# Optimization experiments

Hardware: AMD Instinct MI355X
Metric: run time of the kernel (lower is better)

Reference implementation:

```python
import jax, jax.numpy as jnp
import numpy as np

GN_EPS = 1e-5
GN_GROUPS = 8
KNN_EPS = 1e-8


def group_norm(x, w, b):
    # x: [B, C, N]
    B, C, N = x.shape
    xg = x.reshape(B, GN_GROUPS, C // GN_GROUPS, N)
    mu = jnp.mean(xg, axis=(2, 3), keepdims=True)
    var = jnp.var(xg, axis=(2, 3), keepdims=True)
    xg = (xg - mu) * jax.lax.rsqrt(var + GN_EPS)
    return xg.reshape(B, C, N) * w[None, :, None] + b[None, :, None]


def swish(x):
    return x * jax.nn.sigmoid(x)


def three_interpolate(points_coords, centers_coords, centers_features):
    # points_coords [B,3,N], centers_coords [B,3,M], centers_features [B,C,M]
    B, _, N = points_coords.shape
    C = centers_features.shape[1]
    p2 = jnp.sum(points_coords ** 2, axis=1)            # [B,N]
    c2 = jnp.sum(centers_coords ** 2, axis=1)           # [B,M]
    cross = jnp.einsum('bdn,bdm->bnm', points_coords, centers_coords)
    dist2 = p2[:, :, None] + c2[:, None, :] - 2.0 * cross  # [B,N,M] squared dists
    neg_d, idx = jax.lax.top_k(-dist2, 3)               # 3 smallest -> [B,N,3]
    d = -neg_d
    w = 1.0 / (d + KNN_EPS)
    w = w / jnp.sum(w, axis=-1, keepdims=True)          # [B,N,3]
    featsT = jnp.swapaxes(centers_features, 1, 2)       # [B,M,C]
    gathered = jnp.take_along_axis(featsT, idx.reshape(B, N * 3, 1), axis=1)
    gathered = gathered.reshape(B, N, 3, C)
    out = jnp.einsum('bnk,bnkc->bcn', w, gathered)      # [B,C,N]
    return out


def setup_inputs() -> dict:
    key = jax.random.key(0)
    ks = jax.random.split(key, 8)
    B, N, M = 8, 8192, 2048
    C_ctr, C_pts, D = 256, 128, 64
    Cin, C1, C2 = C_ctr + C_pts, 256, 256
    return {
        'points_coords': jax.random.normal(ks[0], (B, 3, N), jnp.float32),
        'centers_coords': jax.random.normal(ks[1], (B, 3, M), jnp.float32),
        'centers_features': jax.random.normal(ks[2], (B, C_ctr, M), jnp.float32),
        'points_features': jax.random.normal(ks[3], (B, C_pts, N), jnp.float32),
        'time_emb': jax.random.normal(ks[4], (B, D, 1), jnp.float32),
        'W1': jax.random.normal(ks[5], (C1, Cin), jnp.float32) * (1.0 / np.sqrt(Cin)),
        'b1': jnp.zeros((C1,), jnp.float32),
        'gn1_w': jnp.ones((C1,), jnp.float32),
        'gn1_b': jnp.zeros((C1,), jnp.float32),
        'W2': jax.random.normal(ks[6], (C2, C1), jnp.float32) * (1.0 / np.sqrt(C1)),
        'b2': jnp.zeros((C2,), jnp.float32),
        'gn2_w': jnp.ones((C2,), jnp.float32),
        'gn2_b': jnp.zeros((C2,), jnp.float32),
    }


def reference(points_coords, centers_coords, centers_features, points_features,
              time_emb, W1, b1, gn1_w, gn1_b, W2, b2, gn2_w, gn2_b):
    interp = three_interpolate(points_coords, centers_coords, centers_features)
    x = jnp.concatenate([interp, points_features], axis=1)  # [B, Cin, N]
    # SharedMLP layer 1: Conv1d(k=1) + GroupNorm(8) + Swish
    x = jnp.einsum('oc,bcn->bon', W1, x) + b1[None, :, None]
    x = swish(group_norm(x, gn1_w, gn1_b))
    # layer 2
    x = jnp.einsum('oc,bcn->bon', W2, x) + b2[None, :, None]
    x = swish(group_norm(x, gn2_w, gn2_b))
    N = points_coords.shape[-1]
    time_emb_exp = jnp.broadcast_to(time_emb[:, :, 0:1], time_emb.shape[:2] + (N,))
    return (x, points_coords, time_emb_exp)
```

## Files before the change

kernel.cpp:

```cpp
#include <hip/hip_runtime.h>
#include <hip/hip_bf16.h>
#include <float.h>

#define B_ 8
#define N_ 8192
#define M_ 2048
#define CC_ 256
#define CP_ 128
#define CIN_ 384
#define GRP_ 8

typedef __attribute__((ext_vector_type(8))) short short8;
typedef __attribute__((ext_vector_type(4))) short short4v;
typedef __attribute__((ext_vector_type(4))) float f32x4;

static __device__ __forceinline__ float bf2f(unsigned short u) {
  union { unsigned int i; float f; } v; v.i = ((unsigned int)u) << 16; return v.f;
}
static __device__ __forceinline__ unsigned short f2bf(float f) {
  union { float f; unsigned int i; } v; v.f = f;
  unsigned int u = v.i;
  unsigned int r = (u + 0x7FFFu + ((u >> 16) & 1u)) >> 16;
  return (unsigned short)r;
}
static __device__ __forceinline__ void gload16(const void* g, void* l) {
  __builtin_amdgcn_global_load_lds(
      (const __attribute__((address_space(1))) void*)g,
      (__attribute__((address_space(3))) void*)l, 16, 0, 0);
}

__global__ __launch_bounds__(256) void k_prep(
    const float* __restrict__ W1, const float* __restrict__ W2,
    short* __restrict__ W1b, short* __restrict__ W2b,
    const float* __restrict__ cf, short* __restrict__ FT,
    const float* __restrict__ pf, short* __restrict__ x0T) {
  __shared__ float tile[32][33];
  int bid = blockIdx.x;
  int t = threadIdx.x;
  if (bid < 384) {
    int i = bid * 256 + t;
    if (i < 256 * CIN_) W1b[i] = (short)f2bf(W1[i]);
    if (i < 256 * 256)  W2b[i] = (short)f2bf(W2[i]);
    return;
  }
  const float* in; short* out;
  int C, Nn, RS, coff, n0, c0, b;
  if (bid < 4480) {
    int q = bid - 384;
    in = cf; out = FT; C = CC_; Nn = M_; RS = CC_; coff = 0;
    n0 = (q & 63) * 32; c0 = ((q >> 6) & 7) * 32; b = q >> 9;
  } else {
    int q = bid - 4480;
    in = pf; out = x0T; C = CP_; Nn = N_; RS = CIN_; coff = 256;
    n0 = (q & 255) * 32; c0 = ((q >> 8) & 3) * 32; b = q >> 10;
  }
  const float* inb = in + (size_t)b * C * Nn;
  short* outb = out + (size_t)b * Nn * RS;
  int tx = t & 31, ty = t >> 5;
#pragma unroll
  for (int i = 0; i < 32; i += 8)
    tile[ty + i][tx] = inb[(size_t)(c0 + ty + i) * Nn + n0 + tx];
  __syncthreads();
#pragma unroll
  for (int i = 0; i < 32; i += 8)
    outb[(size_t)(n0 + ty + i) * RS + coff + c0 + tx] = (short)f2bf(tile[tx][ty + i]);
}

__global__ __launch_bounds__(256) void k_knn(
    const float* __restrict__ pc, const float* __restrict__ cc,
    int* __restrict__ idx, float* __restrict__ wts) {
  __shared__ __align__(16) float4 ctr[M_];
  __shared__ double mk[4][3][64];
  int b = blockIdx.y;
  int t = threadIdx.x;
  const float* ccb = cc + (size_t)b * 3 * M_;
  for (int i = t; i < M_; i += 256) {
    float x = ccb[i], y = ccb[M_ + i], z = ccb[2 * M_ + i];
    ctr[i] = make_float4(x, y, z, x * x + y * y + z * z);
  }
  __syncthreads();
  int wv = t >> 6, lane = t & 63;
  int n = blockIdx.x * 64 + lane;
  const float* pcb = pc + (size_t)b * 3 * N_;
  float px = pcb[n], py = pcb[N_ + n], pz = pcb[2 * N_ + n];
  float p2 = px * px + py * py + pz * pz;
  double k0 = __hiloint2double(0x7F7FFFFF, 0);
  double k1 = k0, k2 = k0;
  const float4* C = ctr + wv * 512;
  int mbase = wv * 512;
#pragma unroll 8
  for (int m = 0; m < 512; ++m) {
    float4 c = C[m];
    float dot = px * c.x;
    dot = __builtin_fmaf(py, c.y, dot);
    dot = __builtin_fmaf(pz, c.z, dot);
    float d = __builtin_fmaf(-2.f, dot, c.w) + p2;
    double key = __hiloint2double(__float_as_int(d), mbase + m);
    double n0 = fmin(key, k0);
    double n1 = fmin(fmax(key, k0), k1);
    double n2 = fmin(fmax(key, k1), k2);
    k0 = n0; k1 = n1; k2 = n2;
  }
  mk[wv][0][lane] = k0; mk[wv][1][lane] = k1; mk[wv][2][lane] = k2;
  __syncthreads();
  if (t < 64) {
#pragma unroll
    for (int w = 1; w < 4; ++w) {
#pragma unroll
      for (int j = 0; j < 3; ++j) {
        double key = mk[w][j][t];
        double n0 = fmin(key, k0);
        double n1 = fmin(fmax(key, k0), k1);
        double n2 = fmin(fmax(key, k1), k2);
        k0 = n0; k1 = n1; k2 = n2;
      }
    }
    float d0 = __int_as_float(__double2hiint(k0));
    float d1 = __int_as_float(__double2hiint(k1));
    float d2 = __int_as_float(__double2hiint(k2));
    float w0 = 1.f / (d0 + 1e-8f), w1 = 1.f / (d1 + 1e-8f), w2 = 1.f / (d2 + 1e-8f);
    float inv = 1.f / (w0 + w1 + w2);
    int bn = b * N_ + blockIdx.x * 64 + t;
    wts[bn] = w0 * inv; wts[B_ * N_ + bn] = w1 * inv; wts[2 * B_ * N_ + bn] = w2 * inv;
    idx[bn] = __double2loint(k0);
    idx[B_ * N_ + bn] = __double2loint(k1);
    idx[2 * B_ * N_ + bn] = __double2loint(k2);
  }
}

__global__ __launch_bounds__(256) void k_interp(
    const short* __restrict__ FT, const int* __restrict__ idx,
    const float* __restrict__ wts, short* __restrict__ x0T) {
  int b = blockIdx.y;
  int t = threadIdx.x;
  int nl = t >> 5, cch = (t & 31) * 8;
  int n = blockIdx.x * 8 + nl;
  int bn = b * N_ + n;
  int i0 = idx[bn], i1 = idx[B_ * N_ + bn], i2 = idx[2 * B_ * N_ + bn];
  float w0 = wts[bn], w1 = wts[B_ * N_ + bn], w2 = wts[2 * B_ * N_ + bn];
  const short* Fb = FT + (size_t)b * M_ * CC_;
  short8 f0 = *(const short8*)(Fb + (size_t)i0 * CC_ + cch);
  short8 f1 = *(const short8*)(Fb + (size_t)i1 * CC_ + cch);
  short8 f2 = *(const short8*)(Fb + (size_t)i2 * CC_ + cch);
  short8 r;
#pragma unroll
  for (int e = 0; e < 8; ++e) {
    float v = w0 * bf2f((unsigned short)f0[e]) + w1 * bf2f((unsigned short)f1[e]) +
              w2 * bf2f((unsigned short)f2[e]);
    r[e] = (short)f2bf(v);
  }
  *(short8*)(x0T + (size_t)bn * CIN_ + cch) = r;
}

__global__ __launch_bounds__(256) void k_gemm(
    const short* __restrict__ Wb, const short* __restrict__ Xb,
    const float* __restrict__ bias, short* __restrict__ Yb,
    float* __restrict__ part, int K) {
  __shared__ __align__(16) short sW[128 * 64];
  __shared__ __align__(16) short sX[128 * 64];
  int b = blockIdx.z;
  int otile = blockIdx.x * 128;
  int ntile = blockIdx.y * 128;
  int t = threadIdx.x;
  int wv = t >> 6, lane = t & 63;
  int wr = wv >> 1, wc = wv & 1;
  int fr = lane & 15;
  int g = lane >> 4;
  f32x4 acc[4][4] = {};
  const short* Wp = Wb + (size_t)otile * K;
  const short* Xp = Xb + ((size_t)b * N_ + ntile) * K;
  for (int k0 = 0; k0 < K; k0 += 64) {
#pragma unroll
    for (int j = 0; j < 4; ++j) {
      int s = j * 256 + t;
      int row = s >> 3;
      int kc = (s & 7) ^ (row & 7);
      gload16(Wp + (size_t)row * K + k0 + kc * 8, sW + j * 2048 + wv * 512);
      gload16(Xp + (size_t)row * K + k0 + kc * 8, sX + j * 2048 + wv * 512);
    }
    __syncthreads();
#pragma unroll
    for (int h = 0; h < 2; ++h) {
      short8 af[4], bfr[4];
#pragma unroll
      for (int m = 0; m < 4; ++m) {
        int ra = wr * 64 + m * 16 + fr;
        af[m] = *(const short8*)(sW + ra * 64 + (((h * 4 + g) ^ (ra & 7)) << 3));
        int rb = wc * 64 + m * 16 + fr;
        bfr[m] = *(const short8*)(sX + rb * 64 + (((h * 4 + g) ^ (rb & 7)) << 3));
      }
#pragma unroll
      for (int m = 0; m < 4; ++m)
#pragma unroll
        for (int nn = 0; nn < 4; ++nn)
          acc[m][nn] = __builtin_amdgcn_mfma_f32_16x16x32_bf16(af[m], bfr[nn], acc[m][nn], 0, 0, 0);
    }
    __syncthreads();
  }
  float s01 = 0.f, ss01 = 0.f, s23 = 0.f, ss23 = 0.f;
#pragma unroll
  for (int m = 0; m < 4; ++m) {
    int o = otile + wr * 64 + m * 16 + g * 4;
    float4 bi = *(const float4*)(bias + o);
#pragma unroll
    for (int nn = 0; nn < 4; ++nn) {
      int n = ntile + wc * 64 + nn * 16 + fr;
      float v0 = acc[m][nn][0] + bi.x;
      float v1 = acc[m][nn][1] + bi.y;
      float v2 = acc[m][nn][2] + bi.z;
      float v3 = acc[m][nn][3] + bi.w;
      if (m < 2) { s01 += v0 + v1 + v2 + v3; ss01 += v0*v0 + v1*v1 + v2*v2 + v3*v3; }
      else       { s23 += v0 + v1 + v2 + v3; ss23 += v0*v0 + v1*v1 + v2*v2 + v3*v3; }
      short4v sv;
      sv[0] = (short)f2bf(v0);
      sv[1] = (short)f2bf(v1);
      sv[2] = (short)f2bf(v2);
      sv[3] = (short)f2bf(v3);
      *(short4v*)(Yb + ((size_t)b * N_ + n) * 256 + o) = sv;
    }
  }
#pragma unroll
  for (int off = 32; off > 0; off >>= 1) {
    s01 += __shfl_down(s01, off);
    ss01 += __shfl_down(ss01, off);
    s23 += __shfl_down(s23, off);
    ss23 += __shfl_down(ss23, off);
  }
  float* wred = (float*)sW;
  if (lane == 0) {
    wred[wv * 4 + 0] = s01; wred[wv * 4 + 1] = ss01;
    wred[wv * 4 + 2] = s23; wred[wv * 4 + 3] = ss23;
  }
  __syncthreads();
  if (t < 8) {
    int gl = t >> 1, sel = t & 1;
    int wrn = gl >> 1;
    int id = (gl & 1) * 2 + sel;
    float v = wred[(wrn * 2 + 0) * 4 + id] + wred[(wrn * 2 + 1) * 4 + id];
    part[(((size_t)b * 8 + blockIdx.x * 4 + gl) * 64 + blockIdx.y) * 2 + sel] = v;
  }
}

__global__ __launch_bounds__(256) void k_gnapply(short* __restrict__ Y,
                                                 const float* __restrict__ part,
                                                 const float* __restrict__ gw,
                                                 const float* __restrict__ gb) {
  __shared__ float fs[128];
  int t = threadIdx.x;
  if (t < 64) {
    float s = 0.f, ss = 0.f;
    for (int j = 0; j < 64; ++j) {
      s += part[((size_t)t * 64 + j) * 2];
      ss += part[((size_t)t * 64 + j) * 2 + 1];
    }
    const float cnt = 32.f * 8192.f;
    float mean = s / cnt;
    float var = ss / cnt - mean * mean;
    fs[t * 2] = mean;
    fs[t * 2 + 1] = rsqrtf(var + 1e-5f);
  }
  __syncthreads();
  unsigned int* Yd = (unsigned int*)Y;
  int total = B_ * N_ * 128;
  for (int i = blockIdx.x * blockDim.x + t; i < total;
       i += gridDim.x * blockDim.x) {
    int o2 = i & 127;
    int b = i >> 20;
    int g = o2 >> 4;
    float mean = fs[(b * 8 + g) * 2], rstd = fs[(b * 8 + g) * 2 + 1];
    unsigned int v = Yd[i];
    int o = o2 * 2;
    float a = bf2f((unsigned short)(v & 0xFFFF));
    float c = bf2f((unsigned short)(v >> 16));
    a = (a - mean) * rstd * gw[o] + gb[o];
    c = (c - mean) * rstd * gw[o + 1] + gb[o + 1];
    a = a / (1.f + __expf(-a));
    c = c / (1.f + __expf(-c));
    Yd[i] = (unsigned int)f2bf(a) | ((unsigned int)f2bf(c) << 16);
  }
}

__global__ __launch_bounds__(256) void k_gnapply_out(
    const short* __restrict__ Y, const float* __restrict__ part,
    const float* __restrict__ gw, const float* __restrict__ gb,
    float* __restrict__ out) {
  __shared__ float tile[64][65];
  __shared__ float fs[16];
  int b = blockIdx.z;
  int t = threadIdx.x;
  if (t < 8) {
    float s = 0.f, ss = 0.f;
    for (int j = 0; j < 64; ++j) {
      s += part[(((size_t)b * 8 + t) * 64 + j) * 2];
      ss += part[(((size_t)b * 8 + t) * 64 + j) * 2 + 1];
    }
    const float cnt = 32.f * 8192.f;
    float mean = s / cnt;
    float var = ss / cnt - mean * mean;
    fs[t * 2] = mean;
    fs[t * 2 + 1] = rsqrtf(var + 1e-5f);
  }
  __syncthreads();
  int n0 = blockIdx.x * 64, o0 = blockIdx.y * 64;
  int row = t >> 5, dcol = t & 31;
  const unsigned int* Yd = (const unsigned int*)(Y + (size_t)b * N_ * 256);
  int o = o0 + dcol * 2;
  int g = o >> 5;
  float mean = fs[g * 2], rstd = fs[g * 2 + 1];
  float w0 = gw[o], w1 = gw[o + 1], bb0 = gb[o], bb1 = gb[o + 1];
#pragma unroll
  for (int p = 0; p < 8; ++p) {
    int n = n0 + p * 8 + row;
    unsigned int v = Yd[(size_t)n * 128 + (o0 >> 1) + dcol];
    float a = bf2f((unsigned short)(v & 0xFFFF));
    float c = bf2f((unsigned short)(v >> 16));
    a = (a - mean) * rstd * w0 + bb0; a = a / (1.f + __expf(-a));
    c = (c - mean) * rstd * w1 + bb1; c = c / (1.f + __expf(-c));
    tile[p * 8 + row][dcol * 2] = a;
    tile[p * 8 + row][dcol * 2 + 1] = c;
  }
  __syncthreads();
  int ol = t >> 2, nch = (t & 3) * 16;
  float* ob = out + ((size_t)(b * 256 + o0 + ol)) * N_ + n0 + nch;
#pragma unroll
  for (int c4 = 0; c4 < 16; c4 += 4) {
    float4 v4;
    v4.x = tile[nch + c4 + 0][ol];
    v4.y = tile[nch + c4 + 1][ol];
    v4.z = tile[nch + c4 + 2][ol];
    v4.w = tile[nch + c4 + 3][ol];
    *(float4*)(ob + c4) = v4;
  }
}

__global__ void k_tail(const float* __restrict__ pc, const float* __restrict__ te,
                       float* __restrict__ out) {
  int total = 196608 + B_ * 64 * N_;
  for (int i = blockIdx.x * blockDim.x + threadIdx.x; i < total;
       i += gridDim.x * blockDim.x) {
    if (i < 196608) {
      out[16777216 + i] = pc[i];
    } else {
      int j = i - 196608;
      int bd = j >> 13;
      out[16973824 + j] = te[bd];
    }
  }
}

extern "C" void kernel_launch(void* const* d_in, const int* in_sizes, int n_in,
                              void* d_out, int out_size, void* d_ws, size_t ws_size,
                              hipStream_t stream) {
  const float* pc  = (const float*)d_in[0];
  const float* cc  = (const float*)d_in[1];
  const float* cf  = (const float*)d_in[2];
  const float* pf  = (const float*)d_in[3];
  const float* te  = (const float*)d_in[4];
  const float* W1  = (const float*)d_in[5];
  const float* b1  = (const float*)d_in[6];
  const float* g1w = (const float*)d_in[7];
  const float* g1b = (const float*)d_in[8];
  const float* W2  = (const float*)d_in[9];
  const float* b2  = (const float*)d_in[10];
  const float* g2w = (const float*)d_in[11];
  const float* g2b = (const float*)d_in[12];
  float* out = (float*)d_out;

  char* ws = (char*)d_ws;
  size_t off = 0;
  auto alloc = [&](size_t bytes) {
    char* p = ws + off;
    off += (bytes + 255) & ~(size_t)255;
    return p;
  };
  short* FT   = (short*)alloc((size_t)B_ * M_ * CC_ * 2);
  short* x0T  = (short*)alloc((size_t)B_ * N_ * CIN_ * 2);
  short* y1   = (short*)alloc((size_t)B_ * N_ * 256 * 2);
  short* W1b  = (short*)alloc(256 * 384 * 2);
  short* W2b  = (short*)alloc(256 * 256 * 2);
  int*   idx  = (int*)alloc((size_t)3 * B_ * N_ * 4);
  float* wts  = (float*)alloc((size_t)3 * B_ * N_ * 4);
  float* part1 = (float*)alloc(8 * 8 * 64 * 2 * 4);
  float* part2 = (float*)alloc(8 * 8 * 64 * 2 * 4);
  short* y2 = (short*)x0T;

  k_prep<<<12672, 256, 0, stream>>>(W1, W2, W1b, W2b, cf, FT, pf, x0T);
  k_knn<<<dim3(N_ / 64, B_), 256, 0, stream>>>(pc, cc, idx, wts);
  k_interp<<<dim3(N_ / 8, B_), 256, 0, stream>>>(FT, idx, wts, x0T);
  k_gemm<<<dim3(2, N_ / 128, B_), 256, 0, stream>>>(W1b, x0T, b1, y1, part1, CIN_);
  k_gnapply<<<2048, 256, 0, stream>>>(y1, part1, g1w, g1b);
  k_gemm<<<dim3(2, N_ / 128, B_), 256, 0, stream>>>(W2b, y1, b2, y2, part2, 256);
  k_gnapply_out<<<dim3(N_ / 64, 4, B_), 256, 0, stream>>>(y2, part2, g2w, g2b, out);
  k_tail<<<2048, 256, 0, stream>>>(pc, te, out);
}
```

Before: 203.8 us.

## Process two query points per thread in KNN with 8-wave center split

The KNN kernel now handles 128 query points per block with 512 threads, and each thread tracks two independent query points. This lets every LDS center load be reused twice and gives two independent min/max dependency chains for more instruction-level parallelism. The centers are split across 8 waves of 256 each, and the final merge reduces 8 partial top-3 lists per point. The costs are more registers per thread, fewer blocks (512 instead of 1024), and a longer serial merge step.

```diff
diff --git a/kernel.cpp b/kernel.cpp
--- a/kernel.cpp
+++ b/kernel.cpp
@@ -66,46 +66,61 @@
     outb[(size_t)(n0 + ty + i) * RS + coff + c0 + tx] = (short)f2bf(tile[tx][ty + i]);
 }
 
-__global__ __launch_bounds__(256) void k_knn(
+__global__ __launch_bounds__(512) void k_knn(
     const float* __restrict__ pc, const float* __restrict__ cc,
     int* __restrict__ idx, float* __restrict__ wts) {
   __shared__ __align__(16) float4 ctr[M_];
-  __shared__ double mk[4][3][64];
+  __shared__ double mk[8][3][128];
   int b = blockIdx.y;
   int t = threadIdx.x;
   const float* ccb = cc + (size_t)b * 3 * M_;
-  for (int i = t; i < M_; i += 256) {
+  for (int i = t; i < M_; i += 512) {
     float x = ccb[i], y = ccb[M_ + i], z = ccb[2 * M_ + i];
     ctr[i] = make_float4(x, y, z, x * x + y * y + z * z);
   }
   __syncthreads();
   int wv = t >> 6, lane = t & 63;
-  int n = blockIdx.x * 64 + lane;
+  int base = blockIdx.x * 128;
   const float* pcb = pc + (size_t)b * 3 * N_;
-  float px = pcb[n], py = pcb[N_ + n], pz = pcb[2 * N_ + n];
-  float p2 = px * px + py * py + pz * pz;
-  double k0 = __hiloint2double(0x7F7FFFFF, 0);
-  double k1 = k0, k2 = k0;
-  const float4* C = ctr + wv * 512;
-  int mbase = wv * 512;
+  int na = base + lane, nb = base + 64 + lane;
+  float pxa = pcb[na], pya = pcb[N_ + na], pza = pcb[2 * N_ + na];
+  float pxb = pcb[nb], pyb = pcb[N_ + nb], pzb = pcb[2 * N_ + nb];
+  float p2a = pxa * pxa + pya * pya + pza * pza;
+  float p2b = pxb * pxb + pyb * pyb + pzb * pzb;
+  const double kinit = __hiloint2double(0x7F7FFFFF, 0);
+  double a0 = kinit, a1 = kinit, a2 = kinit;
+  double e0 = kinit, e1 = kinit, e2 = kinit;
+  const float4* C = ctr + wv * 256;
+  int mbase = wv * 256;
 #pragma unroll 8
-  for (int m = 0; m < 512; ++m) {
+  for (int m = 0; m < 256; ++m) {
     float4 c = C[m];
-    float dot = px * c.x;
-    dot = __builtin_fmaf(py, c.y, dot);
-    dot = __builtin_fmaf(pz, c.z, dot);
-    float d = __builtin_fmaf(-2.f, dot, c.w) + p2;
-    double key = __hiloint2double(__float_as_int(d), mbase + m);
-    double n0 = fmin(key, k0);
-    double n1 = fmin(fmax(key, k0), k1);
-    double n2 = fmin(fmax(key, k1), k2);
-    k0 = n0; k1 = n1; k2 = n2;
-  }
-  mk[wv][0][lane] = k0; mk[wv][1][lane] = k1; mk[wv][2][lane] = k2;
-  __syncthreads();
-  if (t < 64) {
-#pragma unroll
-    for (int w = 1; w < 4; ++w) {
+    float dota = pxa * c.x;
+    dota = __builtin_fmaf(pya, c.y, dota);
+    dota = __builtin_fmaf(pza, c.z, dota);
+    float da = __builtin_fmaf(-2.f, dota, c.w) + p2a;
+    float dotb = pxb * c.x;
+    dotb = __builtin_fmaf(pyb, c.y, dotb);
+    dotb = __builtin_fmaf(pzb, c.z, dotb);
+    float db = __builtin_fmaf(-2.f, dotb, c.w) + p2b;
+    double ka = __hiloint2double(__float_as_int(da), mbase + m);
+    double kb = __hiloint2double(__float_as_int(db), mbase + m);
+    double t0 = fmin(ka, a0);
+    double t1 = fmin(fmax(ka, a0), a1);
+    double t2 = fmin(fmax(ka, a1), a2);
+    a0 = t0; a1 = t1; a2 = t2;
+    double u0 = fmin(kb, e0);
+    double u1 = fmin(fmax(kb, e0), e1);
+    double u2 = fmin(fmax(kb, e1), e2);
+    e0 = u0; e1 = u1; e2 = u2;
+  }
+  mk[wv][0][lane] = a0; mk[wv][1][lane] = a1; mk[wv][2][lane] = a2;
+  mk[wv][0][64 + lane] = e0; mk[wv][1][64 + lane] = e1; mk[wv][2][64 + lane] = e2;
+  __syncthreads();
+  if (t < 128) {
+    double k0 = kinit, k1 = kinit, k2 = kinit;
+#pragma unroll
+    for (int w = 0; w < 8; ++w) {
 #pragma unroll
       for (int j = 0; j < 3; ++j) {
         double key = mk[w][j][t];
@@ -120,7 +135,7 @@
     float d2 = __int_as_float(__double2hiint(k2));
     float w0 = 1.f / (d0 + 1e-8f), w1 = 1.f / (d1 + 1e-8f), w2 = 1.f / (d2 + 1e-8f);
     float inv = 1.f / (w0 + w1 + w2);
-    int bn = b * N_ + blockIdx.x * 64 + t;
+    int bn = b * N_ + base + t;
     wts[bn] = w0 * inv; wts[B_ * N_ + bn] = w1 * inv; wts[2 * B_ * N_ + bn] = w2 * inv;
     idx[bn] = __double2loint(k0);
     idx[B_ * N_ + bn] = __double2loint(k1);
@@ -385,7 +400,7 @@
   short* y2 = (short*)x0T;
 
   k_prep<<<12672, 256, 0, stream>>>(W1, W2, W1b, W2b, cf, FT, pf, x0T);
-  k_knn<<<dim3(N_ / 64, B_), 256, 0, stream>>>(pc, cc, idx, wts);
+  k_knn<<<dim3(N_ / 128, B_), 512, 0, stream>>>(pc, cc, idx, wts);
   k_interp<<<dim3(N_ / 8, B_), 256, 0, stream>>>(FT, idx, wts, x0T);
   k_gemm<<<dim3(2, N_ / 128, B_), 256, 0, stream>>>(W1b, x0T, b1, y1, part1, CIN_);
   k_gnapply<<<2048, 256, 0, stream>>>(y1, part1, g1w, g1b);
```

Result: faster. 194.8 us (-4.4%).
